# Performance work log

Measured on AMD Instinct MI355X. Metric: run time of the kernel, lower is better.

Reference implementation:

```python
import jax, jax.numpy as jnp
import numpy as np

SAMPLE_SIZE = 8192
K = 8
N_SPLATS = 1_000_000
EPS = 1e-12  # keeps sqrt grad finite on zero-distance (duplicate) pairs


def setup_inputs() -> dict:
    key = jax.random.key(0)
    k1, k2, k3 = jax.random.split(key, 3)
    means = jax.random.normal(k1, (N_SPLATS, 3), dtype=jnp.float32)
    sh0 = jax.random.normal(k2, (N_SPLATS, 1, 3), dtype=jnp.float32)
    idx = jax.random.randint(k3, (SAMPLE_SIZE,), 0, N_SPLATS, dtype=jnp.int64)
    return {"means": means, "sh0": sh0, "idx": idx}


def reference(means, sh0, idx):
    sh0 = sh0.squeeze(1)                    # [N, 3]
    sm = means[idx]                         # [S, 3] sampled positions
    ss = sh0[idx]                           # [S, 3] sampled colors
    # pairwise euclidean distances (torch.cdist, p=2): [S, S]
    sq = jnp.sum(sm * sm, axis=-1)
    d2 = sq[:, None] + sq[None, :] - 2.0 * (sm @ sm.T)
    dist = jnp.sqrt(jnp.maximum(d2, EPS))
    # k+1 smallest per row; drop self (column 0)
    _, knn_idx = jax.lax.top_k(-dist, K + 1)           # [S, K+1]
    knn_idx = knn_idx[:, 1:]                           # [S, K]
    neighbors_sh0 = ss[knn_idx]                        # [S, K, 3]
    neighbor_dist = jnp.take_along_axis(dist, knn_idx, axis=1)[..., None]  # [S, K, 1]
    weight = jnp.exp(-neighbor_dist)
    diff = ss[:, None, :] - neighbors_sh0              # [S, K, 3]
    return jnp.mean(weight * diff * diff)
```

## Files before the change

kernel.cpp:

```cpp
#include <hip/hip_runtime.h>
#include <float.h>
#include <math.h>

#define NSAMPLE 8192
#define KSEL 9
#define KNN 8
#define BLK 512
#define EPS_F 1e-12f

#define ROWS_PB 8
#define NBLOCKS (NSAMPLE / ROWS_PB)
#define RPT 4
#define LANES 64
#define KQT 32
#define BNDI 8
#define BATCH 4
#define WCAP 32
#define BP 257
#define IDX_MASK 0x1FFFu
#define VAL_MASK 0xFFFFE000u
#define PROW 73
#define SROW 289
#define SCALE (1.0f / (float)(NSAMPLE * KNN * 3))

__device__ __forceinline__ unsigned umn(unsigned a, unsigned b) { return a < b ? a : b; }
__device__ __forceinline__ unsigned umx(unsigned a, unsigned b) { return a > b ? a : b; }

__device__ __forceinline__ void insert9(unsigned s[KSEL], unsigned x)
{
#pragma unroll
    for (int k = 0; k < KSEL - 1; ++k)
        s[k] = umx(s[k + 1], umn(x, s[k]));
    s[KSEL - 1] = umn(x, s[KSEL - 1]);
}

__device__ __forceinline__ unsigned pack_d2(float d2, int gidx)
{
    return (__float_as_uint(fmaxf(d2, 0.0f)) & VAL_MASK) | (unsigned)gidx;
}

__global__ __launch_bounds__(256) void gather_k(
    const float* __restrict__ means, const float* __restrict__ sh0,
    const int* __restrict__ idx,
    float4* __restrict__ sm4, float4* __restrict__ ss4)
{
    int i = blockIdx.x * 256 + threadIdx.x;
    if (i >= NSAMPLE) return;
    int id = idx[i];
    const float* m = means + 3 * id;
    const float* s = sh0 + 3 * id;
    float mx = m[0], my = m[1], mz = m[2];
    sm4[i] = make_float4(mx, my, mz, fmaf(mx, mx, fmaf(my, my, mz * mz)));
    ss4[i] = make_float4(s[0], s[1], s[2], 0.0f);
}

__global__ __launch_bounds__(BLK, 8) void main_k(
    const float4* __restrict__ sm4, const float4* __restrict__ ss4,
    float* __restrict__ partial)
{
    __shared__ unsigned wl[8 * RPT * WCAP];
    __shared__ unsigned wcnt[8 * RPT];
    __shared__ unsigned scratch[ROWS_PB * SROW];
    __shared__ unsigned bpart[ROWS_PB * BP];
    __shared__ unsigned partS[ROWS_PB * PROW];
    __shared__ unsigned bnd[ROWS_PB];
    __shared__ float    red[ROWS_PB];

    const int t = threadIdx.x;
    const int lane = t & (LANES - 1);
    const int w = t >> 6;
    const int rpar = w & 1;
    const int quarter = w >> 1;
    const unsigned long long lmask_lt = (1ull << lane) - 1ull;

    float cX[RPT], cY[RPT], cZ[RPT], cW[RPT];
#pragma unroll
    for (int i = 0; i < RPT; ++i) {
        float4 p = sm4[blockIdx.x * ROWS_PB + rpar + 2 * i];
        cX[i] = -2.0f * p.x; cY[i] = -2.0f * p.y; cZ[i] = -2.0f * p.z;
        cW[i] = p.w;
    }

    {
        unsigned pm[RPT];
#pragma unroll
        for (int i = 0; i < RPT; ++i) pm[i] = 0xFFFFFFFFu;
        const int b0 = quarter * (BNDI * LANES);
#pragma unroll
        for (int k = 0; k < BNDI; ++k) {
            const int ci = b0 + k * LANES + lane;
            float4 q = sm4[ci];
#pragma unroll
            for (int i = 0; i < RPT; ++i) {
                float d2 = fmaf(cX[i], q.x,
                           fmaf(cY[i], q.y, fmaf(cZ[i], q.z, cW[i] + q.w)));
                pm[i] = umn(pm[i], pack_d2(d2, ci));
            }
        }
#pragma unroll
        for (int i = 0; i < RPT; ++i)
            bpart[(rpar + 2 * i) * BP + quarter * LANES + lane] = pm[i];
    }
    __syncthreads();

    if (t < 256) {
        const int r1 = t & (ROWS_PB - 1);
        const int g = t >> 3;
        unsigned s[KSEL];
#pragma unroll
        for (int k = 0; k < KSEL; ++k) s[k] = 0xFFFFFFFFu;
#pragma unroll
        for (int e = 0; e < 8; ++e)
            insert9(s, bpart[r1 * BP + g * 8 + e]);
#pragma unroll
        for (int k = 0; k < KSEL; ++k)
            scratch[r1 * SROW + g * KSEL + k] = s[k];
    }
    __syncthreads();
    if (t < 64) {
        const int r1 = t & (ROWS_PB - 1);
        const int mg = t >> 3;
        unsigned m[KSEL];
#pragma unroll
        for (int k = 0; k < KSEL; ++k) m[k] = 0xFFFFFFFFu;
#pragma unroll
        for (int e = 0; e < 4 * KSEL; ++e)
            insert9(m, scratch[r1 * SROW + (4 * mg) * KSEL + e]);
#pragma unroll
        for (int k = 0; k < KSEL; ++k)
            partS[r1 * PROW + mg * KSEL + k] = m[k];
    }
    __syncthreads();
    if (t < ROWS_PB) {
        unsigned m[KSEL];
#pragma unroll
        for (int k = 0; k < KSEL; ++k) m[k] = 0xFFFFFFFFu;
#pragma unroll
        for (int e = 0; e < 8 * KSEL; ++e)
            insert9(m, partS[t * PROW + e]);
        bnd[t] = m[0];
    }
    __syncthreads();

    float bf[RPT];
#pragma unroll
    for (int i = 0; i < RPT; ++i)
        bf[i] = __uint_as_float(bnd[rpar + 2 * i] | IDX_MASK);

    unsigned base[RPT];
#pragma unroll
    for (int i = 0; i < RPT; ++i) base[i] = 0u;

    const int s0 = quarter * (KQT * LANES);
    for (int k0 = 0; k0 < KQT; k0 += BATCH) {
        float4 qr[BATCH];
#pragma unroll
        for (int u = 0; u < BATCH; ++u)
            qr[u] = sm4[s0 + (k0 + u) * LANES + lane];
#pragma unroll
        for (int u = 0; u < BATCH; ++u) {
            const int ci = s0 + (k0 + u) * LANES + lane;
            float d2[RPT];
#pragma unroll
            for (int i = 0; i < RPT; ++i)
                d2[i] = fmaf(cX[i], qr[u].x,
                        fmaf(cY[i], qr[u].y,
                        fmaf(cZ[i], qr[u].z, cW[i] + qr[u].w)));
            float mrg = d2[0] - bf[0];
#pragma unroll
            for (int i = 1; i < RPT; ++i)
                mrg = fminf(mrg, d2[i] - bf[i]);
            if (__any(mrg <= 0.0f)) {
#pragma unroll
                for (int i = 0; i < RPT; ++i) {
                    bool c = (d2[i] <= bf[i]);
                    unsigned long long mk = __ballot(c);
                    if (mk) {
                        unsigned pos = base[i] +
                            (unsigned)__popcll(mk & lmask_lt);
                        if (c && pos < WCAP)
                            wl[(w * RPT + i) * WCAP + pos] = pack_d2(d2[i], ci);
                        base[i] += (unsigned)__popcll(mk);
                    }
                }
            }
        }
    }
    if (lane == 0) {
#pragma unroll
        for (int i = 0; i < RPT; ++i)
            wcnt[w * RPT + i] = umn(base[i], WCAP);
    }
    __syncthreads();

    if (t < 32) {
        const int r1 = t & (ROWS_PB - 1);
        const int q = t >> 3;
        const int wv = 2 * q + (r1 & 1);
        const int li = wv * RPT + (r1 >> 1);
        const unsigned n = wcnt[li];
        unsigned s[KSEL];
#pragma unroll
        for (int k = 0; k < KSEL; ++k) s[k] = 0xFFFFFFFFu;
        for (unsigned k = 0; k < n; ++k)
            insert9(s, wl[li * WCAP + k]);
#pragma unroll
        for (int k = 0; k < KSEL; ++k)
            partS[r1 * PROW + q * KSEL + k] = s[k];
    }
    __syncthreads();

    if (t < ROWS_PB) {
        unsigned m[KSEL];
#pragma unroll
        for (int k = 0; k < KSEL; ++k) m[k] = 0xFFFFFFFFu;
#pragma unroll
        for (int e = 0; e < 4 * KSEL; ++e)
            insert9(m, partS[t * PROW + e]);

        const int gr = blockIdx.x * ROWS_PB + t;
        float4 pm4 = sm4[gr];
        float4 ps4 = ss4[gr];
        float acc = 0.0f;
#pragma unroll
        for (int k = 0; k < KNN; ++k) {
            int j = (int)(m[k] & IDX_MASK);
            float4 qm = sm4[j];
            float dx = pm4.x - qm.x, dy = pm4.y - qm.y, dz = pm4.z - qm.z;
            float d2 = fmaf(dx, dx, fmaf(dy, dy, dz * dz));
            float d = sqrtf(fmaxf(d2, EPS_F));
            float wgt = expf(-d);
            float4 qs = ss4[j];
            float ax = ps4.x - qs.x, ay = ps4.y - qs.y, az = ps4.z - qs.z;
            acc += wgt * (ax * ax + ay * ay + az * az);
        }
        red[t] = acc;
    }
    __syncthreads();
    if (t == 0) {
        float ssum = 0.0f;
#pragma unroll
        for (int i = 0; i < ROWS_PB; ++i) ssum += red[i];
        partial[blockIdx.x] = ssum;
    }
}

__global__ __launch_bounds__(256) void reduce_k(
    const float* __restrict__ partial, float* __restrict__ out)
{
    __shared__ float sbuf[4];
    int t = threadIdx.x;
    float v = 0.0f;
    for (int i = t; i < NBLOCKS; i += 256) v += partial[i];
    for (int off = 32; off > 0; off >>= 1) v += __shfl_down(v, off);
    if ((t & 63) == 0) sbuf[t >> 6] = v;
    __syncthreads();
    if (t == 0) {
        float s = sbuf[0] + sbuf[1] + sbuf[2] + sbuf[3];
        out[0] = s * SCALE;
    }
}

extern "C" void kernel_launch(void* const* d_in, const int* in_sizes, int n_in,
                              void* d_out, int out_size, void* d_ws, size_t ws_size,
                              hipStream_t stream)
{
    const float* means = (const float*)d_in[0];
    const float* sh0   = (const float*)d_in[1];
    const int*   idxp  = (const int*)d_in[2];

    float4* sm4 = (float4*)d_ws;
    float4* ss4 = sm4 + NSAMPLE;
    float*  partial = (float*)(ss4 + NSAMPLE);

    gather_k<<<NSAMPLE / 256, 256, 0, stream>>>(means, sh0, idxp, sm4, ss4);
    main_k<<<NBLOCKS, BLK, 0, stream>>>(sm4, ss4, partial);
    reduce_k<<<1, 256, 0, stream>>>(partial, (float*)d_out);
}
```

Baseline: 103.4 us.

## Double-buffer candidate loads and scalarize row constants in KNN filter loop

The candidate scan now double-buffers its float4 loads so the next batch is fetched while the current batch is compared. Row constants are forced into scalar registers with readfirstlane. The per-row squared norm is folded into a precomputed threshold, with a small relative slack so the comparison still accepts every true candidate, which removes one add per distance. The any-vote precheck is replaced by four ballots, and the prefix popcount now uses mbcnt. The slack may let a few extra candidates into the worklist, and the worklist is capped at WCAP entries.

```diff
diff --git a/kernel.cpp b/kernel.cpp
--- a/kernel.cpp
+++ b/kernel.cpp
@@ -39,6 +39,18 @@
     return (__float_as_uint(fmaxf(d2, 0.0f)) & VAL_MASK) | (unsigned)gidx;
 }
 
+__device__ __forceinline__ float sfl(float x)
+{
+    return __uint_as_float((unsigned)__builtin_amdgcn_readfirstlane(
+        (int)__float_as_uint(x)));
+}
+
+__device__ __forceinline__ unsigned mbcnt64(unsigned long long m)
+{
+    return __builtin_amdgcn_mbcnt_hi((unsigned)(m >> 32),
+           __builtin_amdgcn_mbcnt_lo((unsigned)(m & 0xFFFFFFFFull), 0u));
+}
+
 __global__ __launch_bounds__(256) void gather_k(
     const float* __restrict__ means, const float* __restrict__ sh0,
     const int* __restrict__ idx,
@@ -54,6 +66,35 @@
     ss4[i] = make_float4(s[0], s[1], s[2], 0.0f);
 }
 
+#define PROCESS(QR, KB)                                                       \
+    {                                                                         \
+        _Pragma("unroll")                                                     \
+        for (int u = 0; u < BATCH; ++u) {                                     \
+            float sv[RPT];                                                    \
+            _Pragma("unroll")                                                 \
+            for (int i = 0; i < RPT; ++i)                                     \
+                sv[i] = fmaf(cX[i], QR[u].x, fmaf(cY[i], QR[u].y,             \
+                        fmaf(cZ[i], QR[u].z, QR[u].w)));                      \
+            unsigned long long mk[RPT];                                       \
+            _Pragma("unroll")                                                 \
+            for (int i = 0; i < RPT; ++i)                                     \
+                mk[i] = __ballot(sv[i] <= sb[i]);                             \
+            if (mk[0] | mk[1] | mk[2] | mk[3]) {                              \
+                const int ci = s0 + ((KB) + u) * LANES + lane;                \
+                _Pragma("unroll")                                             \
+                for (int i = 0; i < RPT; ++i) {                               \
+                    if (mk[i]) {                                              \
+                        unsigned pos = base[i] + mbcnt64(mk[i]);              \
+                        if ((sv[i] <= sb[i]) && pos < WCAP)                   \
+                            wl[(w * RPT + i) * WCAP + pos] =                  \
+                                pack_d2(sv[i] + cW[i], ci);                   \
+                        base[i] += (unsigned)__popcll(mk[i]);                 \
+                    }                                                         \
+                }                                                             \
+            }                                                                 \
+        }                                                                     \
+    }
+
 __global__ __launch_bounds__(BLK, 8) void main_k(
     const float4* __restrict__ sm4, const float4* __restrict__ ss4,
     float* __restrict__ partial)
@@ -71,14 +112,15 @@
     const int w = t >> 6;
     const int rpar = w & 1;
     const int quarter = w >> 1;
-    const unsigned long long lmask_lt = (1ull << lane) - 1ull;
 
     float cX[RPT], cY[RPT], cZ[RPT], cW[RPT];
 #pragma unroll
     for (int i = 0; i < RPT; ++i) {
         float4 p = sm4[blockIdx.x * ROWS_PB + rpar + 2 * i];
-        cX[i] = -2.0f * p.x; cY[i] = -2.0f * p.y; cZ[i] = -2.0f * p.z;
-        cW[i] = p.w;
+        cX[i] = sfl(-2.0f * p.x);
+        cY[i] = sfl(-2.0f * p.y);
+        cZ[i] = sfl(-2.0f * p.z);
+        cW[i] = sfl(p.w);
     }
 
     {
@@ -92,9 +134,9 @@
             float4 q = sm4[ci];
 #pragma unroll
             for (int i = 0; i < RPT; ++i) {
-                float d2 = fmaf(cX[i], q.x,
-                           fmaf(cY[i], q.y, fmaf(cZ[i], q.z, cW[i] + q.w)));
-                pm[i] = umn(pm[i], pack_d2(d2, ci));
+                float s = fmaf(cX[i], q.x,
+                          fmaf(cY[i], q.y, fmaf(cZ[i], q.z, q.w)));
+                pm[i] = umn(pm[i], pack_d2(s + cW[i], ci));
             }
         }
 #pragma unroll
@@ -142,49 +184,36 @@
     }
     __syncthreads();
 
-    float bf[RPT];
-#pragma unroll
-    for (int i = 0; i < RPT; ++i)
-        bf[i] = __uint_as_float(bnd[rpar + 2 * i] | IDX_MASK);
+    float sb[RPT];
+#pragma unroll
+    for (int i = 0; i < RPT; ++i) {
+        float bfv = __uint_as_float(bnd[rpar + 2 * i] | IDX_MASK);
+        float D = bfv - cW[i];
+        sb[i] = sfl(D + (bfv + fabsf(D)) * 6.0e-7f + 1e-33f);
+    }
 
     unsigned base[RPT];
 #pragma unroll
     for (int i = 0; i < RPT; ++i) base[i] = 0u;
 
     const int s0 = quarter * (KQT * LANES);
-    for (int k0 = 0; k0 < KQT; k0 += BATCH) {
-        float4 qr[BATCH];
+    const float4* __restrict__ qp = sm4 + s0 + lane;
+
+    float4 qa[BATCH], qb[BATCH];
+#pragma unroll
+    for (int u = 0; u < BATCH; ++u) qa[u] = qp[u * LANES];
+
+    for (int k0 = 0; k0 < KQT; k0 += 2 * BATCH) {
 #pragma unroll
         for (int u = 0; u < BATCH; ++u)
-            qr[u] = sm4[s0 + (k0 + u) * LANES + lane];
-#pragma unroll
-        for (int u = 0; u < BATCH; ++u) {
-            const int ci = s0 + (k0 + u) * LANES + lane;
-            float d2[RPT];
-#pragma unroll
-            for (int i = 0; i < RPT; ++i)
-                d2[i] = fmaf(cX[i], qr[u].x,
-                        fmaf(cY[i], qr[u].y,
-                        fmaf(cZ[i], qr[u].z, cW[i] + qr[u].w)));
-            float mrg = d2[0] - bf[0];
-#pragma unroll
-            for (int i = 1; i < RPT; ++i)
-                mrg = fminf(mrg, d2[i] - bf[i]);
-            if (__any(mrg <= 0.0f)) {
-#pragma unroll
-                for (int i = 0; i < RPT; ++i) {
-                    bool c = (d2[i] <= bf[i]);
-                    unsigned long long mk = __ballot(c);
-                    if (mk) {
-                        unsigned pos = base[i] +
-                            (unsigned)__popcll(mk & lmask_lt);
-                        if (c && pos < WCAP)
-                            wl[(w * RPT + i) * WCAP + pos] = pack_d2(d2[i], ci);
-                        base[i] += (unsigned)__popcll(mk);
-                    }
-                }
-            }
+            qb[u] = qp[(k0 + BATCH + u) * LANES];
+        PROCESS(qa, k0)
+        if (k0 + 2 * BATCH < KQT) {
+#pragma unroll
+            for (int u = 0; u < BATCH; ++u)
+                qa[u] = qp[(k0 + 2 * BATCH + u) * LANES];
         }
+        PROCESS(qb, k0 + BATCH)
     }
     if (lane == 0) {
 #pragma unroll
```

New measurement: 100.3 us. 3.0% less time.
